# Optimization experiments

Hardware: AMD Instinct MI355X
Metric: run time of the kernel (lower is better)

The kernel has to match this reference:

```python
import jax, jax.numpy as jnp
import numpy as np

B, S, E = 8, 2048, 1024
EPS = 1e-5

def _layernorm(x, w, b):
    mu = jnp.mean(x, axis=-1, keepdims=True)
    var = jnp.mean(jnp.square(x - mu), axis=-1, keepdims=True)
    return (x - mu) * jax.lax.rsqrt(var + EPS) * w + b

def setup_inputs() -> dict:
    key = jax.random.key(0)
    ks = jax.random.split(key, 12)
    x = jax.random.normal(ks[0], (B, S, E), dtype=jnp.float32)
    pad_mask = jax.random.randint(ks[1], (B, 1, S), 0, 2).astype(bool)
    pad_mask = pad_mask.at[:, :, 0].set(False)  # ensure no fully-masked row
    s = 1.0 / np.sqrt(E)
    Wq = jax.random.normal(ks[2], (E, E), jnp.float32) * s
    Wk = jax.random.normal(ks[3], (E, E), jnp.float32) * s
    Wv = jax.random.normal(ks[4], (E, E), jnp.float32) * s
    bq = jnp.zeros((E,), jnp.float32)
    bk = jnp.zeros((E,), jnp.float32)
    bv = jnp.zeros((E,), jnp.float32)
    W1 = jax.random.normal(ks[5], (2 * E, E), jnp.float32) * s
    b1 = jnp.zeros((2 * E,), jnp.float32)
    W2 = jax.random.normal(ks[6], (E, 2 * E), jnp.float32) * (1.0 / np.sqrt(2 * E))
    b2 = jnp.zeros((E,), jnp.float32)
    ln1_w = jnp.ones((E,), jnp.float32); ln1_b = jnp.zeros((E,), jnp.float32)
    ln2_w = jnp.ones((E,), jnp.float32); ln2_b = jnp.zeros((E,), jnp.float32)
    return {"x": x, "pad_mask": pad_mask, "ln1_w": ln1_w, "ln1_b": ln1_b,
            "ln2_w": ln2_w, "ln2_b": ln2_b, "Wq": Wq, "bq": bq, "Wk": Wk,
            "bk": bk, "Wv": Wv, "bv": bv, "W1": W1, "b1": b1, "W2": W2, "b2": b2}

def reference(x, pad_mask, ln1_w, ln1_b, ln2_w, ln2_b, Wq, bq, Wk, bk, Wv, bv, W1, b1, W2, b2):
    scale = jnp.sqrt(jnp.float32(x.shape[-1]))
    normed = _layernorm(x, ln1_w, ln1_b)
    Q = jnp.einsum('bse,de->bsd', normed, Wq) + bq
    K = jnp.einsum('bse,de->bsd', normed, Wk) + bk
    V = jnp.einsum('bse,de->bsd', normed, Wv) + bv
    scores = jnp.einsum('bqd,bkd->bqk', Q, K) / scale  # [B,S,S]
    scores = jnp.where(pad_mask, -jnp.inf, scores)
    attn = jax.nn.softmax(scores, axis=2)  # dropout is identity at inference
    x = x + jnp.einsum('bqk,bkd->bqd', attn, V)
    h = _layernorm(x, ln2_w, ln2_b)
    h = jax.nn.relu(jnp.einsum('bse,fe->bsf', h, W1) + b1)
    x = x + jnp.einsum('bsf,ef->bse', h, W2) + b2
    return x
```

## Files before the change

### kernel.cpp

```cpp
#include <hip/hip_runtime.h>
#include <hip/hip_bf16.h>
#include <cstdint>

#define B_ 8
#define S_ 2048
#define E_ 1024

using u16 = unsigned short;

typedef __bf16 bf16x8 __attribute__((ext_vector_type(8)));
typedef float f32x4 __attribute__((ext_vector_type(4)));

__device__ inline u16 f2bf(float f) {
  uint32_t u = __float_as_uint(f);
  uint32_t r = (u + 0x7fffu + ((u >> 16) & 1u)) >> 16;
  return (u16)r;
}

template<bool HAS_BIAS, bool RELU, bool HAS_RES, bool OUT_BF16, bool SCORES,
         bool GATHER_A, bool RUNTK>
__global__ __launch_bounds__(512, 2) void gemm_nt(
    const u16* __restrict__ A, const u16* __restrict__ B, void* __restrict__ C,
    const float* __restrict__ bias, const float* __restrict__ res,
    int lda, int ldb, int ldc, int K,
    long long strideA, long long strideB, long long strideC,
    const int* __restrict__ cidx, const int* __restrict__ cnt)
{
  __shared__ __attribute__((aligned(16))) u16 lA[2][2][128 * 64];
  __shared__ __attribute__((aligned(16))) u16 lB[2][2][128 * 64];

  const int tid  = threadIdx.x;
  const int lane = tid & 63;
  const int wave = tid >> 6;

  const int GM = 8, GN = 4;
  const int nbn = gridDim.x, nbm = gridDim.y, nz = gridDim.z;
  int bm, bn, bz;
  {
    const int total = nbn * nbm * nz;
    const long long lin = blockIdx.x +
        (long long)nbn * (blockIdx.y + (long long)nbm * blockIdx.z);
    if ((nbm % GM) == 0 && (nbn % GN) == 0 && (total % (8 * GM * GN)) == 0) {
      const int xcd = (int)(lin & 7);
      const int loc = (int)(lin >> 3);
      const int sper = GM * GN;
      const int super = (loc / sper) * 8 + xcd;
      const int ins   = loc % sper;
      const int spz = (nbm / GM) * (nbn / GN);
      bz = super / spz;
      const int s2 = super % spz;
      const int sm = s2 % (nbm / GM);
      const int sn = s2 / (nbm / GM);
      bm = sm * GM + (ins % GM);
      bn = sn * GN + (ins / GM);
    } else { bm = blockIdx.y; bn = blockIdx.x; bz = blockIdx.z; }
  }

  int count = 0, cpad = 0;
  if (SCORES || GATHER_A || RUNTK) {
    count = cnt[bz * 2];
    cpad  = cnt[bz * 2 + 1];
    if (GATHER_A && bm * 256 >= cpad) return;
    if (SCORES   && bn * 256 >= cpad) return;
  }
  const int Keff = RUNTK ? cpad : K;
  const int nk = Keff >> 6;

  const u16* Ab = A + (long long)bz * strideA;
  const u16* Bb = B + (long long)bz * strideB;

  const int srow = tid >> 3;
  const int scol = ((tid & 7) ^ (srow & 7)) * 8;
  long long rowA[2][2], rowB[2][2];
#pragma unroll
  for (int h = 0; h < 2; ++h)
#pragma unroll
    for (int l = 0; l < 2; ++l) {
      int ra = bm * 256 + h * 128 + srow + l * 64;
      if (GATHER_A) ra = cidx[(long long)bz * S_ + ra];
      rowA[h][l] = (long long)ra * lda + scol;
      rowB[h][l] = (long long)(bn * 256 + h * 128 + srow + l * 64) * ldb + scol;
    }
  const int ldsoff0 = tid * 8;
  const int ldsoff1 = (tid + 512) * 8;

  const int wr = wave >> 2, wc = wave & 3;
  const int rA = wr * 64 + (lane & 15);
  const int rB = wc * 32 + (lane & 15);
#define LDSP3(P) ((uint32_t)(uintptr_t)(__attribute__((address_space(3))) const void*)(P))
  uint32_t aA0 = LDSP3(&lA[0][0][0]) +
      2u * (uint32_t)(rA * 64 + (((0 * 4 + (lane >> 4)) ^ (rA & 7)) * 8));
  uint32_t aA1 = LDSP3(&lA[0][0][0]) +
      2u * (uint32_t)(rA * 64 + (((1 * 4 + (lane >> 4)) ^ (rA & 7)) * 8));
  uint32_t bB0 = LDSP3(&lB[0][0][0]) +
      2u * (uint32_t)(rB * 64 + (((0 * 4 + (lane >> 4)) ^ (rB & 7)) * 8));
  uint32_t bB1 = LDSP3(&lB[0][0][0]) +
      2u * (uint32_t)(rB * 64 + (((1 * 4 + (lane >> 4)) ^ (rB & 7)) * 8));
#undef LDSP3

  f32x4 acc[2][2][4][2];
#pragma unroll
  for (int a = 0; a < 2; ++a)
#pragma unroll
    for (int b = 0; b < 2; ++b)
#pragma unroll
      for (int mi = 0; mi < 4; ++mi)
#pragma unroll
        for (int ni = 0; ni < 2; ++ni)
          acc[a][b][mi][ni] = (f32x4){0.f, 0.f, 0.f, 0.f};

#define STAGE_A(H, T) {                                                        \
    const int tt_ = ((T) < nk) ? (T) : (nk - 1);                               \
    __builtin_amdgcn_global_load_lds(                                          \
        (const __attribute__((address_space(1))) void*)                        \
            (Ab + rowA[H][0] + (long long)tt_ * 64),                           \
        (__attribute__((address_space(3))) void*)(&lA[(T) & 1][H][ldsoff0]),   \
        16, 0, 0);                                                             \
    __builtin_amdgcn_global_load_lds(                                          \
        (const __attribute__((address_space(1))) void*)                        \
            (Ab + rowA[H][1] + (long long)tt_ * 64),                           \
        (__attribute__((address_space(3))) void*)(&lA[(T) & 1][H][ldsoff1]),   \
        16, 0, 0); }

#define STAGE_B(H, T) {                                                        \
    const int tt_ = ((T) < nk) ? (T) : (nk - 1);                               \
    __builtin_amdgcn_global_load_lds(                                          \
        (const __attribute__((address_space(1))) void*)                        \
            (Bb + rowB[H][0] + (long long)tt_ * 64),                           \
        (__attribute__((address_space(3))) void*)(&lB[(T) & 1][H][ldsoff0]),   \
        16, 0, 0);                                                             \
    __builtin_amdgcn_global_load_lds(                                          \
        (const __attribute__((address_space(1))) void*)                        \
            (Bb + rowB[H][1] + (long long)tt_ * 64),                           \
        (__attribute__((address_space(3))) void*)(&lB[(T) & 1][H][ldsoff1]),   \
        16, 0, 0); }

#define DSR(D, ADDR, OFF) \
    asm volatile("ds_read_b128 %0, %1 offset:" OFF : "=v"(D) : "v"(ADDR))

#define LGKM(NSTR) asm volatile("s_waitcnt lgkmcnt(" NSTR ")" ::: "memory")
#define SCHED0()   __builtin_amdgcn_sched_barrier(0)
#define BAR()      __builtin_amdgcn_s_barrier()

#define MFMA_MI(MH, NH, MI, BF) {                                              \
    _Pragma("unroll") for (int ni = 0; ni < 2; ++ni)                           \
      _Pragma("unroll") for (int k2 = 0; k2 < 2; ++k2)                         \
        acc[MH][NH][MI][ni] = __builtin_amdgcn_mfma_f32_16x16x32_bf16(         \
            af[MI][k2], BF[ni][k2], acc[MH][NH][MI][ni], 0, 0, 0); }

  STAGE_A(0, 0); STAGE_B(0, 0); STAGE_B(1, 0); STAGE_A(1, 0);
  STAGE_B(0, 1); STAGE_B(1, 1); STAGE_A(0, 1); STAGE_A(1, 1);
  asm volatile("s_waitcnt vmcnt(8)" ::: "memory");
  BAR();

  bf16x8 af[4][2], bfv[2][2], bfv2[2][2];
  for (int t = 0; t < nk; ++t) {
    DSR(af[0][0], aA0, "0");      DSR(af[0][1], aA1, "0");
    DSR(bfv[0][0], bB0, "0");     DSR(bfv[0][1], bB1, "0");
    DSR(bfv[1][0], bB0, "2048");  DSR(bfv[1][1], bB1, "2048");
    DSR(af[1][0], aA0, "2048");   DSR(af[1][1], aA1, "2048");
    DSR(af[2][0], aA0, "4096");   DSR(af[2][1], aA1, "4096");
    DSR(af[3][0], aA0, "6144");   DSR(af[3][1], aA1, "6144");
    DSR(bfv2[0][0], bB0, "16384"); DSR(bfv2[0][1], bB1, "16384");
    DSR(bfv2[1][0], bB0, "18432"); DSR(bfv2[1][1], bB1, "18432");
    BAR();
    __builtin_amdgcn_s_setprio(1);
    LGKM("10"); SCHED0(); MFMA_MI(0, 0, 0, bfv);
    LGKM("8");  SCHED0(); MFMA_MI(0, 0, 1, bfv);
    LGKM("6");  SCHED0(); MFMA_MI(0, 0, 2, bfv);
    LGKM("0");  SCHED0(); MFMA_MI(0, 0, 3, bfv);
    __builtin_amdgcn_s_setprio(0);
    BAR();
    STAGE_B(0, t + 2); STAGE_B(1, t + 2);
    BAR();
    __builtin_amdgcn_s_setprio(1);
    MFMA_MI(0, 1, 0, bfv2); MFMA_MI(0, 1, 1, bfv2);
    MFMA_MI(0, 1, 2, bfv2); MFMA_MI(0, 1, 3, bfv2);
    __builtin_amdgcn_s_setprio(0);
    BAR();
    DSR(af[0][0], aA0, "16384"); DSR(af[0][1], aA1, "16384");
    DSR(af[1][0], aA0, "18432"); DSR(af[1][1], aA1, "18432");
    DSR(af[2][0], aA0, "20480"); DSR(af[2][1], aA1, "20480");
    DSR(af[3][0], aA0, "22528"); DSR(af[3][1], aA1, "22528");
    STAGE_A(0, t + 2);
    BAR();
    __builtin_amdgcn_s_setprio(1);
    LGKM("6"); SCHED0(); MFMA_MI(1, 1, 0, bfv2);
    LGKM("4"); SCHED0(); MFMA_MI(1, 1, 1, bfv2);
    LGKM("2"); SCHED0(); MFMA_MI(1, 1, 2, bfv2);
    LGKM("0"); SCHED0(); MFMA_MI(1, 1, 3, bfv2);
    __builtin_amdgcn_s_setprio(0);
    BAR();
    STAGE_A(1, t + 2);
    BAR();
    __builtin_amdgcn_s_setprio(1);
    MFMA_MI(1, 0, 0, bfv); MFMA_MI(1, 0, 1, bfv);
    MFMA_MI(1, 0, 2, bfv); MFMA_MI(1, 0, 3, bfv);
    __builtin_amdgcn_s_setprio(0);
    asm volatile("s_waitcnt vmcnt(8)" ::: "memory");
    BAR();
    const uint32_t d = (t & 1) ? (uint32_t)-32768 : 32768u;
    aA0 += d; aA1 += d; bB0 += d; bB1 += d;
  }
  asm volatile("s_waitcnt vmcnt(0)" ::: "memory");

#undef MFMA_MI
#undef DSR
#undef STAGE_A
#undef STAGE_B
#undef BAR
#undef LGKM
#undef SCHED0

  const float* resb = (const float*)C;
  if (HAS_RES) resb = res + (long long)bz * strideC;
  u16*   cb16 = (u16*)C   + (long long)bz * strideC;
  float* cf32 = (float*)C + (long long)bz * strideC;

#pragma unroll
  for (int mh = 0; mh < 2; ++mh)
#pragma unroll
  for (int nh = 0; nh < 2; ++nh)
#pragma unroll
  for (int ni = 0; ni < 2; ++ni) {
    const int gn = bn * 256 + nh * 128 + wc * 32 + ni * 16 + (lane & 15);
    const float bvv = HAS_BIAS ? bias[gn] : 0.f;
    const bool cmask = SCORES && (gn >= count);
#pragma unroll
    for (int mi = 0; mi < 4; ++mi) {
#pragma unroll
      for (int r = 0; r < 4; ++r) {
        const int gm = bm * 256 + mh * 128 + wr * 64 + mi * 16 + (lane >> 4) * 4 + r;
        const long long idx = (long long)gm * ldc + gn;
        float v = acc[mh][nh][mi][ni][r] + bvv;
        if (SCORES) { v *= 0.03125f; if (cmask) v = -3.0e38f; }
        if (RELU) v = fmaxf(v, 0.f);
        if (HAS_RES) v += resb[idx];
        if (OUT_BF16) cb16[idx] = f2bf(v);
        else          cf32[idx] = v;
      }
    }
  }
}

__global__ __launch_bounds__(256) void layernorm_kernel(
    const float* __restrict__ x, const float* __restrict__ w,
    const float* __restrict__ b, u16* __restrict__ out)
{
  const int row = blockIdx.x;
  const int tid = threadIdx.x;
  const float4 v = ((const float4*)(x + (long long)row * E_))[tid];
  float s  = v.x + v.y + v.z + v.w;
  float s2 = v.x * v.x + v.y * v.y + v.z * v.z + v.w * v.w;
#pragma unroll
  for (int o = 32; o >= 1; o >>= 1) { s += __shfl_xor(s, o); s2 += __shfl_xor(s2, o); }
  __shared__ float rs[4], rs2[4];
  const int wave = tid >> 6, lane = tid & 63;
  if (lane == 0) { rs[wave] = s; rs2[wave] = s2; }
  __syncthreads();
  s  = rs[0] + rs[1] + rs[2] + rs[3];
  s2 = rs2[0] + rs2[1] + rs2[2] + rs2[3];
  const float mu   = s * (1.f / E_);
  const float var  = s2 * (1.f / E_) - mu * mu;
  const float rstd = rsqrtf(var + 1e-5f);
  const float4 wv = ((const float4*)w)[tid];
  const float4 bv = ((const float4*)b)[tid];
  ushort4 o;
  o.x = f2bf((v.x - mu) * rstd * wv.x + bv.x);
  o.y = f2bf((v.y - mu) * rstd * wv.y + bv.y);
  o.z = f2bf((v.z - mu) * rstd * wv.z + bv.z);
  o.w = f2bf((v.w - mu) * rstd * wv.w + bv.w);
  ((ushort4*)(out + (long long)row * E_))[tid] = o;
}

__global__ __launch_bounds__(256) void softmax_bf16_kernel(
    u16* __restrict__ sp, const int* __restrict__ cnt)
{
  const int row = blockIdx.x;
  const int bz  = row >> 11;
  const int tid = threadIdx.x;
  const int cpad = cnt[bz * 2 + 1];
  const bool act = (tid * 8) < cpad;
  u16* pr = sp + (long long)row * S_;

  float v[8];
  if (act) {
    const uint4 raw = ((const uint4*)pr)[tid];
    const uint32_t w[4] = {raw.x, raw.y, raw.z, raw.w};
#pragma unroll
    for (int c = 0; c < 4; ++c) {
      v[2 * c]     = __uint_as_float(w[c] << 16);
      v[2 * c + 1] = __uint_as_float(w[c] & 0xffff0000u);
    }
  } else {
#pragma unroll
    for (int i = 0; i < 8; ++i) v[i] = -3.38e38f;
  }
  float mx = -3.38e38f;
#pragma unroll
  for (int i = 0; i < 8; ++i) mx = fmaxf(mx, v[i]);
#pragma unroll
  for (int o = 32; o >= 1; o >>= 1) mx = fmaxf(mx, __shfl_xor(mx, o));
  __shared__ float red[4];
  const int wave = tid >> 6, lane = tid & 63;
  if (lane == 0) red[wave] = mx;
  __syncthreads();
  mx = fmaxf(fmaxf(red[0], red[1]), fmaxf(red[2], red[3]));

  float s = 0.f;
#pragma unroll
  for (int i = 0; i < 8; ++i) { v[i] = __expf(v[i] - mx); s += v[i]; }
#pragma unroll
  for (int o = 32; o >= 1; o >>= 1) s += __shfl_xor(s, o);
  __syncthreads();
  if (lane == 0) red[wave] = s;
  __syncthreads();
  s = red[0] + red[1] + red[2] + red[3];
  const float inv = 1.f / s;

  if (act) {
    uint4 o4;
    uint32_t* ow = (uint32_t*)&o4;
#pragma unroll
    for (int c = 0; c < 4; ++c) {
      const uint32_t lo = f2bf(v[2 * c] * inv);
      const uint32_t hi = f2bf(v[2 * c + 1] * inv);
      ow[c] = lo | (hi << 16);
    }
    ((uint4*)pr)[tid] = o4;
  }
}

__global__ __launch_bounds__(256) void transpose_kernel(
    const u16* __restrict__ KVc, u16* __restrict__ Vt, const int* __restrict__ cnt)
{
  const int bl = blockIdx.z;
  const int s0 = blockIdx.y * 32;
  if (s0 >= cnt[bl * 2 + 1]) return;
  __shared__ u16 tile[32][33];
  const int e0 = blockIdx.x * 32;
  const int tx = threadIdx.x & 31, ty = threadIdx.x >> 5;
  const u16* src = KVc + ((long long)bl * S_ + s0) * (2 * E_) + E_ + e0;
#pragma unroll
  for (int r = 0; r < 32; r += 8)
    tile[ty + r][tx] = src[(long long)(ty + r) * (2 * E_) + tx];
  __syncthreads();
  u16* dst = Vt + ((long long)bl * E_ + e0) * S_ + s0;
#pragma unroll
  for (int r = 0; r < 32; r += 8)
    dst[(long long)(ty + r) * S_ + tx] = tile[tx][ty + r];
}

__global__ __launch_bounds__(256) void prep_kernel(
    const float* __restrict__ Wq, const float* __restrict__ Wk,
    const float* __restrict__ Wv, const float* __restrict__ W1,
    const float* __restrict__ W2, const float* __restrict__ bk,
    const float* __restrict__ bv,
    u16* __restrict__ Wqb, u16* __restrict__ Wkvb,
    u16* __restrict__ W1b, u16* __restrict__ W2b, float* __restrict__ bkv)
{
  const int N1 = E_ * E_;
  const long long i = (long long)blockIdx.x * 256 + threadIdx.x;
  if (i < N1)               Wqb[i] = f2bf(Wq[i]);
  else if (i < 2LL * N1)    Wkvb[i - N1] = f2bf(Wk[i - N1]);
  else if (i < 3LL * N1)    Wkvb[N1 + (i - 2LL * N1)] = f2bf(Wv[i - 2LL * N1]);
  else if (i < 5LL * N1)    W1b[i - 3LL * N1] = f2bf(W1[i - 3LL * N1]);
  else if (i < 7LL * N1)    W2b[i - 5LL * N1] = f2bf(W2[i - 5LL * N1]);
  else if (i < 7LL * N1 + 2 * E_) {
    const int j = (int)(i - 7LL * N1);
    bkv[j] = (j < E_) ? bk[j] : bv[j - E_];
  }
}

__global__ void detect_kernel(const unsigned char* __restrict__ m, int* __restrict__ flag)
{
  __shared__ int any;
  if (threadIdx.x == 0) any = 0;
  __syncthreads();
  int loc = 0;
  for (int i = threadIdx.x; i < B_ * S_; i += 256)
    if ((i & 3) && m[i]) loc = 1;
  if (loc) atomicOr(&any, 1);
  __syncthreads();
  if (threadIdx.x == 0) *flag = any;
}

__global__ __launch_bounds__(256) void compact_kernel(
    const void* __restrict__ mask, const int* __restrict__ flag,
    int* __restrict__ cidx, int* __restrict__ cnt)
{
  const int b = blockIdx.x;
  const int tid = threadIdx.x, lane = tid & 63, wave = tid >> 6;
  const bool u8m = (*flag != 0);
  const unsigned char* m8 = (const unsigned char*)mask + (long long)b * S_;
  const int* m32 = (const int*)mask + (long long)b * S_;

  int keep[8]; int my = 0;
#pragma unroll
  for (int j = 0; j < 8; ++j) {
    const int s = tid * 8 + j;
    const bool k = u8m ? (m8[s] == 0) : (m32[s] == 0);
    keep[j] = k ? 1 : 0; my += keep[j];
  }
  int pre = my;
#pragma unroll
  for (int o = 1; o < 64; o <<= 1) {
    const int n = __shfl_up(pre, o);
    if (lane >= o) pre += n;
  }
  __shared__ int wsum[4];
  if (lane == 63) wsum[wave] = pre;
  __syncthreads();
  int wbase = 0;
#pragma unroll
  for (int w = 0; w < 4; ++w) if (w < wave) wbase += wsum[w];
  int pos = wbase + pre - my;
  int* cx = cidx + (long long)b * S_;
#pragma unroll
  for (int j = 0; j < 8; ++j)
    if (keep[j]) cx[pos++] = tid * 8 + j;
  const int total = wsum[0] + wsum[1] + wsum[2] + wsum[3];
  const int cpad = (total + 255) & ~255;
  for (int i = total + tid; i < cpad; i += 256) cx[i] = 0;
  if (tid == 0) { cnt[b * 2] = total; cnt[b * 2 + 1] = cpad; }
}

extern "C" void kernel_launch(void* const* d_in, const int* in_sizes, int n_in,
                              void* d_out, int out_size, void* d_ws, size_t ws_size,
                              hipStream_t stream)
{
  const float* x    = (const float*)d_in[0];
  const void*  mask = d_in[1];
  const float* ln1w = (const float*)d_in[2];
  const float* ln1b = (const float*)d_in[3];
  const float* ln2w = (const float*)d_in[4];
  const float* ln2b = (const float*)d_in[5];
  const float* Wq   = (const float*)d_in[6];
  const float* bq   = (const float*)d_in[7];
  const float* Wk   = (const float*)d_in[8];
  const float* bk   = (const float*)d_in[9];
  const float* Wv   = (const float*)d_in[10];
  const float* bv   = (const float*)d_in[11];
  const float* W1   = (const float*)d_in[12];
  const float* b1   = (const float*)d_in[13];
  const float* W2   = (const float*)d_in[14];
  const float* b2   = (const float*)d_in[15];

  const size_t MB = 1024ull * 1024ull;
  char* p = (char*)d_ws;
  int* flag    = (int*)p;   p += 256;
  int* cnt     = (int*)p;   p += 256;
  int* cidx    = (int*)p;   p += (size_t)B_ * S_ * 4;
  u16* Wqb     = (u16*)p;   p += (size_t)E_ * E_ * 2;
  u16* Wkvb    = (u16*)p;   p += (size_t)2 * E_ * E_ * 2;
  u16* W1b     = (u16*)p;   p += (size_t)2 * E_ * E_ * 2;
  u16* W2b     = (u16*)p;   p += (size_t)2 * E_ * E_ * 2;
  float* bkv   = (float*)p; p += 2 * E_ * 4;
  u16* normedb = (u16*)p;   p += (size_t)B_ * S_ * E_ * 2;
  char* chunk  = p;
  const size_t used  = (size_t)(p - (char*)d_ws);
  const size_t avail = (ws_size > used) ? (ws_size - used) : 0;

  int bc = 1;
  for (int c = 8; c >= 1; c >>= 1)
    if (avail >= 24 * MB * (size_t)c) { bc = c; break; }

  float* out = (float*)d_out;
  dim3 blk(256);
  dim3 blkg(512);

  detect_kernel<<<1, 256, 0, stream>>>((const unsigned char*)mask, flag);
  compact_kernel<<<B_, blk, 0, stream>>>(mask, flag, cidx, cnt);
  {
    const long long tot = 7LL * E_ * E_ + 2 * E_;
    prep_kernel<<<(int)((tot + 255) / 256), blk, 0, stream>>>(
        Wq, Wk, Wv, W1, W2, bk, bv, Wqb, Wkvb, W1b, W2b, bkv);
  }

  layernorm_kernel<<<B_ * S_, blk, 0, stream>>>(x, ln1w, ln1b, normedb);

  for (int b0 = 0; b0 < B_; b0 += bc) {
    u16* Qc  = (u16*)chunk;
    u16* KVc = Qc + (size_t)bc * S_ * E_;
    u16* Vt  = KVc + (size_t)bc * S_ * 2 * E_;
    u16* Pc  = Vt + (size_t)bc * E_ * S_;
    const int* cntb  = cnt + b0 * 2;
    const int* cidxb = cidx + (size_t)b0 * S_;

    gemm_nt<true, false, false, true, false, false, false>
        <<<dim3(E_ / 256, bc * S_ / 256, 1), blkg, 0, stream>>>(
        normedb + (size_t)b0 * S_ * E_, Wqb, Qc, bq, nullptr,
        E_, E_, E_, E_, 0, 0, 0, nullptr, nullptr);

    gemm_nt<true, false, false, true, false, true, false>
        <<<dim3(2 * E_ / 256, S_ / 256, bc), blkg, 0, stream>>>(
        normedb + (size_t)b0 * S_ * E_, Wkvb, KVc, bkv, nullptr,
        E_, E_, 2 * E_, E_,
        (long long)S_ * E_, 0, (long long)S_ * 2 * E_, cidxb, cntb);

    transpose_kernel<<<dim3(E_ / 32, S_ / 32, bc), blk, 0, stream>>>(KVc, Vt, cntb);

    gemm_nt<false, false, false, true, true, false, false>
        <<<dim3(S_ / 256, S_ / 256, bc), blkg, 0, stream>>>(
        Qc, KVc, Pc, nullptr, nullptr,
        E_, 2 * E_, S_, E_,
        (long long)S_ * E_, (long long)S_ * 2 * E_, (long long)S_ * S_,
        nullptr, cntb);

    softmax_bf16_kernel<<<bc * S_, blk, 0, stream>>>(Pc, cntb);

    gemm_nt<false, false, true, false, false, false, true>
        <<<dim3(E_ / 256, S_ / 256, bc), blkg, 0, stream>>>(
        Pc, Vt, out + (size_t)b0 * S_ * E_, nullptr,
        x + (size_t)b0 * S_ * E_, S_, S_, E_, S_,
        (long long)S_ * S_, (long long)E_ * S_, (long long)S_ * E_,
        nullptr, cntb);
  }

  layernorm_kernel<<<B_ * S_, blk, 0, stream>>>(out, ln2w, ln2b, normedb);

  size_t mr_sz = avail / ((size_t)2 * E_ * 2);
  int mr = (int)((mr_sz > 16384) ? 16384 : mr_sz);
  mr &= ~255;
  if (mr < 256) mr = 256;
  u16* hb = (u16*)chunk;
  for (int m0 = 0; m0 < B_ * S_; m0 += mr) {
    const int mm = (B_ * S_ - m0 < mr) ? (B_ * S_ - m0) : mr;
    gemm_nt<true, true, false, true, false, false, false>
        <<<dim3((2 * E_) / 256, mm / 256, 1), blkg, 0, stream>>>(
        normedb + (size_t)m0 * E_, W1b, hb, b1, nullptr,
        E_, E_, 2 * E_, E_, 0, 0, 0, nullptr, nullptr);
    gemm_nt<true, false, true, false, false, false, false>
        <<<dim3(E_ / 256, mm / 256, 1), blkg, 0, stream>>>(
        hb, W2b, out + (size_t)m0 * E_, b2, out + (size_t)m0 * E_,
        2 * E_, 2 * E_, E_, 2 * E_, 0, 0, 0, nullptr, nullptr);
  }
}
```

Measured before the change: 628.4 us.

## Prefetch next-iteration LDS fragments across loop boundary and drop a barrier

Restructures the GEMM main loop so the A and B fragments for the next k-step are read from LDS at the end of the current iteration, overlapping with the final MFMA group and the last A staging load. One barrier phase per iteration is removed, and the precomputed staging address replaces the per-macro clamp computation. The vmcnt wait changes from 8 to 6 to match the reordered loads. The risk is a race or hazard: LDS reads of the next buffer may now overlap with async global_load_lds writes if the wait counts are off.

```diff
diff --git a/kernel.cpp b/kernel.cpp
--- a/kernel.cpp
+++ b/kernel.cpp
@@ -135,9 +135,28 @@
         (__attribute__((address_space(3))) void*)(&lB[(T) & 1][H][ldsoff1]),   \
         16, 0, 0); }
 
+#define STAGE_A2(H) {                                                          \
+    __builtin_amdgcn_global_load_lds(                                          \
+        (const __attribute__((address_space(1))) void*)(Ab + rowA[H][0] + ko2),\
+        (__attribute__((address_space(3))) void*)(lAb + (H) * 8192 + ldsoff0), \
+        16, 0, 0);                                                             \
+    __builtin_amdgcn_global_load_lds(                                          \
+        (const __attribute__((address_space(1))) void*)(Ab + rowA[H][1] + ko2),\
+        (__attribute__((address_space(3))) void*)(lAb + (H) * 8192 + ldsoff1), \
+        16, 0, 0); }
+
+#define STAGE_B2(H) {                                                          \
+    __builtin_amdgcn_global_load_lds(                                          \
+        (const __attribute__((address_space(1))) void*)(Bb + rowB[H][0] + ko2),\
+        (__attribute__((address_space(3))) void*)(lBb + (H) * 8192 + ldsoff0), \
+        16, 0, 0);                                                             \
+    __builtin_amdgcn_global_load_lds(                                          \
+        (const __attribute__((address_space(1))) void*)(Bb + rowB[H][1] + ko2),\
+        (__attribute__((address_space(3))) void*)(lBb + (H) * 8192 + ldsoff1), \
+        16, 0, 0); }
+
 #define DSR(D, ADDR, OFF) \
     asm volatile("ds_read_b128 %0, %1 offset:" OFF : "=v"(D) : "v"(ADDR))
-
 #define LGKM(NSTR) asm volatile("s_waitcnt lgkmcnt(" NSTR ")" ::: "memory")
 #define SCHED0()   __builtin_amdgcn_sched_barrier(0)
 #define BAR()      __builtin_amdgcn_s_barrier()
@@ -154,24 +173,29 @@
   BAR();
 
   bf16x8 af[4][2], bfv[2][2], bfv2[2][2];
+  DSR(af[0][0], aA0, "0");     DSR(af[0][1], aA1, "0");
+  DSR(af[1][0], aA0, "2048");  DSR(af[1][1], aA1, "2048");
+  DSR(af[2][0], aA0, "4096");  DSR(af[2][1], aA1, "4096");
+  DSR(af[3][0], aA0, "6144");  DSR(af[3][1], aA1, "6144");
+  DSR(bfv[0][0], bB0, "0");    DSR(bfv[0][1], bB1, "0");
+  DSR(bfv[1][0], bB0, "2048"); DSR(bfv[1][1], bB1, "2048");
+
   for (int t = 0; t < nk; ++t) {
-    DSR(af[0][0], aA0, "0");      DSR(af[0][1], aA1, "0");
-    DSR(bfv[0][0], bB0, "0");     DSR(bfv[0][1], bB1, "0");
-    DSR(bfv[1][0], bB0, "2048");  DSR(bfv[1][1], bB1, "2048");
-    DSR(af[1][0], aA0, "2048");   DSR(af[1][1], aA1, "2048");
-    DSR(af[2][0], aA0, "4096");   DSR(af[2][1], aA1, "4096");
-    DSR(af[3][0], aA0, "6144");   DSR(af[3][1], aA1, "6144");
+    const int t2 = (t + 2 < nk) ? (t + 2) : (nk - 1);
+    const long long ko2 = (long long)t2 * 64;
+    u16* lAb = &lA[t & 1][0][0];
+    u16* lBb = &lB[t & 1][0][0];
     DSR(bfv2[0][0], bB0, "16384"); DSR(bfv2[0][1], bB1, "16384");
     DSR(bfv2[1][0], bB0, "18432"); DSR(bfv2[1][1], bB1, "18432");
     BAR();
     __builtin_amdgcn_s_setprio(1);
-    LGKM("10"); SCHED0(); MFMA_MI(0, 0, 0, bfv);
-    LGKM("8");  SCHED0(); MFMA_MI(0, 0, 1, bfv);
-    LGKM("6");  SCHED0(); MFMA_MI(0, 0, 2, bfv);
-    LGKM("0");  SCHED0(); MFMA_MI(0, 0, 3, bfv);
+    LGKM("4"); SCHED0();
+    MFMA_MI(0, 0, 0, bfv); MFMA_MI(0, 0, 1, bfv);
+    MFMA_MI(0, 0, 2, bfv); MFMA_MI(0, 0, 3, bfv);
     __builtin_amdgcn_s_setprio(0);
+    LGKM("0");
     BAR();
-    STAGE_B(0, t + 2); STAGE_B(1, t + 2);
+    STAGE_B2(0); STAGE_B2(1);
     BAR();
     __builtin_amdgcn_s_setprio(1);
     MFMA_MI(0, 1, 0, bfv2); MFMA_MI(0, 1, 1, bfv2);
@@ -182,7 +206,7 @@
     DSR(af[1][0], aA0, "18432"); DSR(af[1][1], aA1, "18432");
     DSR(af[2][0], aA0, "20480"); DSR(af[2][1], aA1, "20480");
     DSR(af[3][0], aA0, "22528"); DSR(af[3][1], aA1, "22528");
-    STAGE_A(0, t + 2);
+    STAGE_A2(0);
     BAR();
     __builtin_amdgcn_s_setprio(1);
     LGKM("6"); SCHED0(); MFMA_MI(1, 1, 0, bfv2);
@@ -191,23 +215,35 @@
     LGKM("0"); SCHED0(); MFMA_MI(1, 1, 3, bfv2);
     __builtin_amdgcn_s_setprio(0);
     BAR();
-    STAGE_A(1, t + 2);
-    BAR();
     __builtin_amdgcn_s_setprio(1);
     MFMA_MI(1, 0, 0, bfv); MFMA_MI(1, 0, 1, bfv);
     MFMA_MI(1, 0, 2, bfv); MFMA_MI(1, 0, 3, bfv);
     __builtin_amdgcn_s_setprio(0);
-    asm volatile("s_waitcnt vmcnt(8)" ::: "memory");
-    BAR();
-    const uint32_t d = (t & 1) ? (uint32_t)-32768 : 32768u;
-    aA0 += d; aA1 += d; bB0 += d; bB1 += d;
-  }
-  asm volatile("s_waitcnt vmcnt(0)" ::: "memory");
+    SCHED0();
+    asm volatile("s_waitcnt vmcnt(6)" ::: "memory");
+    {
+      const uint32_t ad = (t & 1) ? (uint32_t)-32768 : 32768u;
+      const uint32_t aA0n = aA0 + ad, aA1n = aA1 + ad;
+      const uint32_t bB0n = bB0 + ad, bB1n = bB1 + ad;
+      DSR(af[0][0], aA0n, "0");     DSR(af[0][1], aA1n, "0");
+      DSR(af[1][0], aA0n, "2048");  DSR(af[1][1], aA1n, "2048");
+      DSR(af[2][0], aA0n, "4096");  DSR(af[2][1], aA1n, "4096");
+      DSR(af[3][0], aA0n, "6144");  DSR(af[3][1], aA1n, "6144");
+      DSR(bfv[0][0], bB0n, "0");    DSR(bfv[0][1], bB1n, "0");
+      DSR(bfv[1][0], bB0n, "2048"); DSR(bfv[1][1], bB1n, "2048");
+      STAGE_A2(1);
+      BAR();
+      aA0 = aA0n; aA1 = aA1n; bB0 = bB0n; bB1 = bB1n;
+    }
+  }
+  asm volatile("s_waitcnt vmcnt(0) lgkmcnt(0)" ::: "memory");
 
 #undef MFMA_MI
 #undef DSR
 #undef STAGE_A
 #undef STAGE_B
+#undef STAGE_A2
+#undef STAGE_B2
 #undef BAR
 #undef LGKM
 #undef SCHED0
```

Result: no change. 624.2 us (-0.7%).
